# Performance work log

Hardware: AMD Instinct MI355X
Metric: run time of the kernel (lower is better)

The kernel has to match this reference:

```python
import jax, jax.numpy as jnp
import numpy as np

N_NODES = 100000
N_EDGES = 1600000
IN_DIM = 128
OUT_DIM = 64
SLOPE = 0.2


def setup_inputs() -> dict:
    key = jax.random.key(0)
    k1, k2, k3, k4 = jax.random.split(key, 4)
    h = jax.random.normal(k1, (N_NODES, IN_DIM), dtype=jnp.float32)
    W = jax.random.normal(k2, (OUT_DIM, IN_DIM), dtype=jnp.float32) * (1.0 / np.sqrt(IN_DIM))
    src = jax.random.randint(k3, (N_EDGES,), 0, N_NODES, dtype=jnp.int64)
    dst = jax.random.randint(k4, (N_EDGES,), 0, N_NODES, dtype=jnp.int64)
    return {"h": h, "W": W, "src": src, "dst": dst}


def reference(h, W, src, dst):
    n = h.shape[0]
    z = h @ W.T                                   # [N, out_dim]
    z_src = z[src]                                # [E, out_dim]
    z_dst = z[dst]                                # [E, out_dim]
    e = jax.nn.leaky_relu(jnp.sum(z_src * z_dst, axis=1), negative_slope=SLOPE)  # [E]
    # segment softmax over incoming edges of each destination node
    m = jax.ops.segment_max(e, dst, num_segments=n)        # [N], -inf for isolated nodes
    ex = jnp.exp(e - m[dst])                                # [E]
    denom = jax.ops.segment_sum(ex, dst, num_segments=n)    # [N]
    alpha = ex / denom[dst]                                 # [E]
    agg = jax.ops.segment_sum(alpha[:, None] * z_src, dst, num_segments=n)  # [N, out_dim]
    return jax.nn.elu(agg)
```

## Files before the change

### kernel.cpp

```cpp
#include <hip/hip_runtime.h>
#include <math.h>

#define SLOPE 0.2f
#define LOG2E 1.4426950408889634f

__global__ __launch_bounds__(256, 8) void gemm_hist_kernel(const float* __restrict__ h,
                                                           const float* __restrict__ W,
                                                           float* __restrict__ z,
                                                           const int* __restrict__ dst,
                                                           int* __restrict__ cnt8,
                                                           unsigned short* __restrict__ rank,
                                                           int n, int ne) {
    int g = blockIdx.x / 3;
    int r = blockIdx.x % 3;
    if (r == 2) {
        int* __restrict__ cnt = cnt8 + (size_t)(g & 7) * n;
        int i = g * 256 + threadIdx.x;
        int base = i * 4;
        if (base + 3 < ne) {
            int4 d = *(const int4*)(dst + base);
            unsigned int r0 = atomicAdd(&cnt[d.x], 1);
            unsigned int r1 = atomicAdd(&cnt[d.y], 1);
            unsigned int r2 = atomicAdd(&cnt[d.z], 1);
            unsigned int r3 = atomicAdd(&cnt[d.w], 1);
            uint2 packed;
            packed.x = (r1 << 16) | (r0 & 0xFFFF);
            packed.y = (r3 << 16) | (r2 & 0xFFFF);
            *(uint2*)(rank + base) = packed;
        } else if (base < ne) {
            for (int rr = base; rr < ne; rr++)
                rank[rr] = (unsigned short)atomicAdd(&cnt[dst[rr]], 1);
        }
        return;
    }

    __shared__ float ws[128][36];
    int t = threadIdx.x;
    int gemmIdx = 2 * g + r;
    int nblk = gemmIdx >> 1;
    int ch0  = (gemmIdx & 1) << 5;
    const float4* __restrict__ W4 = reinterpret_cast<const float4*>(W);
#pragma unroll
    for (int j = 0; j < 4; j++) {
        int idx = t + j * 256;
        int o  = idx >> 5;
        int kq = idx & 31;
        float4 w = W4[(size_t)(ch0 + o) * 32 + kq];
        int k = kq << 2;
        int col = o ^ ((kq & 7) << 2);
        ws[k + 0][col] = w.x; ws[k + 1][col] = w.y;
        ws[k + 2][col] = w.z; ws[k + 3][col] = w.w;
    }
    __syncthreads();

    int ng = t >> 3, og = t & 7;
    int n0 = nblk * 64 + ng * 2;
    if (n0 >= n) return;
    const float* __restrict__ hp = h + (size_t)n0 * 128;

    float acc[2][4] = {};
#pragma unroll 4
    for (int k = 0; k < 128; k += 4) {
        int m = (k >> 2) & 7;
        int colb = (og ^ m) << 2;
        float4 hv[2], wv[4];
#pragma unroll
        for (int i = 0; i < 2; i++) hv[i] = *(const float4*)(hp + i * 128 + k);
#pragma unroll
        for (int kk = 0; kk < 4; kk++) wv[kk] = *(const float4*)&ws[k + kk][colb];
#pragma unroll
        for (int i = 0; i < 2; i++) {
            acc[i][0] += hv[i].x * wv[0].x + hv[i].y * wv[1].x + hv[i].z * wv[2].x + hv[i].w * wv[3].x;
            acc[i][1] += hv[i].x * wv[0].y + hv[i].y * wv[1].y + hv[i].z * wv[2].y + hv[i].w * wv[3].y;
            acc[i][2] += hv[i].x * wv[0].z + hv[i].y * wv[1].z + hv[i].z * wv[2].z + hv[i].w * wv[3].z;
            acc[i][3] += hv[i].x * wv[0].w + hv[i].y * wv[1].w + hv[i].z * wv[2].w + hv[i].w * wv[3].w;
        }
    }
#pragma unroll
    for (int i = 0; i < 2; i++) {
        *(float4*)&z[(size_t)(n0 + i) * 64 + ch0 + og * 4] =
            make_float4(acc[i][0], acc[i][1], acc[i][2], acc[i][3]);
    }
}

__global__ __launch_bounds__(256) void scan1(const int* __restrict__ cnt8,
                                             int* __restrict__ starts,
                                             int* __restrict__ bsums, int n) {
    __shared__ int ls[256];
    int tbase = blockIdx.x * 4096 + threadIdx.x * 16;
    int tot[16];
#pragma unroll
    for (int k = 0; k < 16; k++) tot[k] = 0;
    if (tbase + 15 < n) {
#pragma unroll
        for (int c = 0; c < 8; c++) {
            const int* cp = cnt8 + (size_t)c * n + tbase;
#pragma unroll
            for (int q = 0; q < 4; q++) {
                int4 v = *(const int4*)(cp + q * 4);
                tot[q * 4 + 0] += v.x; tot[q * 4 + 1] += v.y;
                tot[q * 4 + 2] += v.z; tot[q * 4 + 3] += v.w;
            }
        }
    } else {
        for (int k = 0; k < 16; k++) {
            int idx = tbase + k;
            if (idx < n)
                for (int c = 0; c < 8; c++) tot[k] += cnt8[(size_t)c * n + idx];
        }
    }
    int s = 0;
#pragma unroll
    for (int k = 0; k < 16; k++) s += tot[k];
    ls[threadIdx.x] = s;
    __syncthreads();
    for (int off = 1; off < 256; off <<= 1) {
        int t = threadIdx.x >= off ? ls[threadIdx.x - off] : 0;
        __syncthreads();
        ls[threadIdx.x] += t;
        __syncthreads();
    }
    int run = ls[threadIdx.x] - s;
    if (threadIdx.x == 255) bsums[blockIdx.x] = ls[255];
#pragma unroll
    for (int k = 0; k < 16; k++) {
        int idx = tbase + k;
        if (idx < n) starts[idx] = run;
        run += tot[k];
    }
}

__global__ __launch_bounds__(256) void scan3(int* __restrict__ starts,
                                             const int* __restrict__ bsums,
                                             int* __restrict__ cnt8,
                                             int n, int ne) {
    __shared__ int base_s;
    int i = blockIdx.x * 256 + threadIdx.x;
    if (threadIdx.x == 0) {
        int reg = (int)(blockIdx.x >> 4);
        int s = 0;
        for (int b = 0; b < reg; b++) s += bsums[b];
        base_s = s;
        if (blockIdx.x == 0) starts[n] = ne;
    }
    __syncthreads();
    if (i >= n) return;
    int b = starts[i] + base_s;
    starts[i] = b;
#pragma unroll
    for (int c = 0; c < 8; c++) {
        size_t off = (size_t)c * n + i;
        int t = cnt8[off];
        cnt8[off] = b;
        b += t;
    }
}

__global__ __launch_bounds__(256) void scatter8_kernel(const int* __restrict__ src,
                                                       const int* __restrict__ dst,
                                                       const int* __restrict__ cnt8,
                                                       const unsigned short* __restrict__ rank,
                                                       int* __restrict__ csr_src,
                                                       int n, int ne) {
    int i = blockIdx.x * 256 + threadIdx.x;
    int base = i * 8;
    if (base + 7 < ne) {
        const int* __restrict__ cb = cnt8 + (size_t)((base >> 10) & 7) * n;
        int4 s0 = *(const int4*)(src + base),  s1 = *(const int4*)(src + base + 4);
        int4 d0 = *(const int4*)(dst + base),  d1 = *(const int4*)(dst + base + 4);
        uint4 rp = *(const uint4*)(rank + base);
        csr_src[cb[d0.x] + (rp.x & 0xFFFF)] = s0.x;
        csr_src[cb[d0.y] + (rp.x >> 16)]    = s0.y;
        csr_src[cb[d0.z] + (rp.y & 0xFFFF)] = s0.z;
        csr_src[cb[d0.w] + (rp.y >> 16)]    = s0.w;
        csr_src[cb[d1.x] + (rp.z & 0xFFFF)] = s1.x;
        csr_src[cb[d1.y] + (rp.z >> 16)]    = s1.y;
        csr_src[cb[d1.z] + (rp.w & 0xFFFF)] = s1.z;
        csr_src[cb[d1.w] + (rp.w >> 16)]    = s1.w;
    } else {
        for (int e = base; e < ne; e++) {
            const int* cb = cnt8 + (size_t)((e >> 10) & 7) * n;
            csr_src[cb[dst[e]] + rank[e]] = src[e];
        }
    }
}

__global__ __launch_bounds__(256) void fused_node(const float4* __restrict__ z4,
                                                  const int* __restrict__ starts,
                                                  const int* __restrict__ csr_src,
                                                  float4* __restrict__ out4, int n) {
    int node = blockIdx.x * 4 + (threadIdx.x >> 6);
    if (node >= n) return;
    int lane = threadIdx.x & 63;
    int g = lane >> 4;
    int q = lane & 15;
    int rs = starts[node], re = starts[node + 1];
    float4 zd = z4[(size_t)node * 16 + q];

    float m2 = -1e30f, denom = 0.f;
    float4 acc = make_float4(0.f, 0.f, 0.f, 0.f);

    for (int c = rs; c < re; c += 64) {
        int j = c + lane;
        int sv = j < re ? csr_src[j] : 0;
        int cn = min(64, re - c);
        bool val0 = g < cn;
        int  s0 = __shfl(sv, val0 ? g : 0);
        float4 v0 = z4[(size_t)s0 * 16 + q];
        bool val1 = 4 + g < cn;
        int  s1 = __shfl(sv, val1 ? 4 + g : 0);
        float4 v1 = z4[(size_t)s1 * 16 + q];
        for (int k = 0; k < cn; k += 4) {
            int idx2 = k + 8 + g;
            bool val2 = idx2 < cn;
            int  s2 = __shfl(sv, val2 ? idx2 : 0);
            float4 v2 = z4[(size_t)s2 * 16 + q];
            float p = v0.x * zd.x + v0.y * zd.y + v0.z * zd.z + v0.w * zd.w;
#pragma unroll
            for (int msk = 1; msk < 16; msk <<= 1) p += __shfl_xor(p, msk);
            float e = p > 0.f ? p : SLOPE * p;
            float e2 = e * LOG2E;
            e2 = val0 ? e2 : -2e30f;
            if (__any(e2 > m2)) {
                float mnew = fmaxf(m2, e2);
                float sc = exp2f(m2 - mnew);
                float ex = exp2f(e2 - mnew);
                denom = fmaf(denom, sc, ex);
                acc.x = fmaf(acc.x, sc, ex * v0.x);
                acc.y = fmaf(acc.y, sc, ex * v0.y);
                acc.z = fmaf(acc.z, sc, ex * v0.z);
                acc.w = fmaf(acc.w, sc, ex * v0.w);
                m2 = mnew;
            } else {
                float ex = exp2f(e2 - m2);
                denom += ex;
                acc.x = fmaf(ex, v0.x, acc.x);
                acc.y = fmaf(ex, v0.y, acc.y);
                acc.z = fmaf(ex, v0.z, acc.z);
                acc.w = fmaf(ex, v0.w, acc.w);
            }
            v0 = v1; val0 = val1;
            v1 = v2; val1 = val2;
        }
    }
#pragma unroll
    for (int msk = 16; msk < 64; msk <<= 1) {
        float mo  = __shfl_xor(m2, msk);
        float dno = __shfl_xor(denom, msk);
        float ax = __shfl_xor(acc.x, msk);
        float ay = __shfl_xor(acc.y, msk);
        float az = __shfl_xor(acc.z, msk);
        float aw = __shfl_xor(acc.w, msk);
        float mnew = fmaxf(m2, mo);
        float ss = exp2f(m2 - mnew), so = exp2f(mo - mnew);
        denom = fmaf(denom, ss, dno * so);
        acc.x = fmaf(acc.x, ss, ax * so);
        acc.y = fmaf(acc.y, ss, ay * so);
        acc.z = fmaf(acc.z, ss, az * so);
        acc.w = fmaf(acc.w, ss, aw * so);
        m2 = mnew;
    }
    if (lane < 16) {
        float inv = denom > 0.f ? 1.f / denom : 0.f;
        float4 r; float x;
        x = acc.x * inv; r.x = x > 0.f ? x : __expf(x) - 1.f;
        x = acc.y * inv; r.y = x > 0.f ? x : __expf(x) - 1.f;
        x = acc.z * inv; r.z = x > 0.f ? x : __expf(x) - 1.f;
        x = acc.w * inv; r.w = x > 0.f ? x : __expf(x) - 1.f;
        out4[(size_t)node * 16 + q] = r;
    }
}

extern "C" void kernel_launch(void* const* d_in, const int* in_sizes, int n_in,
                              void* d_out, int out_size, void* d_ws, size_t ws_size,
                              hipStream_t stream) {
    const float* h   = (const float*)d_in[0];
    const float* W   = (const float*)d_in[1];
    const int*   src = (const int*)d_in[2];
    const int*   dst = (const int*)d_in[3];
    int n  = in_sizes[0] / 128;
    int ne = in_sizes[2];

    float*          z       = (float*)d_ws;
    unsigned short* rank    = (unsigned short*)(z + (size_t)n * 64);
    int*            cnt8    = (int*)(rank + ne);
    int*            csr_src = cnt8 + (size_t)8 * n;
    int*            starts  = csr_src + ne;
    int*            bsums   = starts + ((n + 5) & ~3);

    int nbHist = (ne / 4 + 255) / 256;
    int nbTotal = nbHist * 3;
    int nb_scan = (n + 4095) / 4096;

    hipMemsetAsync(cnt8, 0, (size_t)8 * n * sizeof(int), stream);
    gemm_hist_kernel<<<nbTotal, 256, 0, stream>>>(h, W, z, dst, cnt8, rank, n, ne);
    scan1<<<nb_scan, 256, 0, stream>>>(cnt8, starts, bsums, n);
    scan3<<<(n + 255) / 256, 256, 0, stream>>>(starts, bsums, cnt8, n, ne);
    scatter8_kernel<<<(ne / 8 + 255) / 256, 256, 0, stream>>>(src, dst, cnt8,
                                                              rank, csr_src, n, ne);
    fused_node<<<(n + 3) / 4, 256, 0, stream>>>((const float4*)z, starts, csr_src,
                                                (float4*)d_out, n);
}
```

Measured before the change: 196.8 us.

## Store projected features as fp16 and gather eight edges per wavefront step

The GEMM now writes z in half precision, halving the bytes of the intermediate feature table. The node kernel gathers 16-byte fp16 rows with 8 lanes per edge, so each wavefront processes 8 edges per iteration instead of 4 and needs fewer shuffle reductions. This targets the gather bandwidth and instruction count of the random edge reads. In exchange it adds conversion work and rounds z to fp16, which may affect accuracy.

```diff
diff --git a/kernel.cpp b/kernel.cpp
--- a/kernel.cpp
+++ b/kernel.cpp
@@ -1,12 +1,21 @@
 #include <hip/hip_runtime.h>
+#include <hip/hip_fp16.h>
 #include <math.h>
 
 #define SLOPE 0.2f
 #define LOG2E 1.4426950408889634f
 
+__device__ __forceinline__ unsigned short pk_f16(float x) {
+    __half h = __float2half(x);
+    return __half_as_ushort(h);
+}
+__device__ __forceinline__ float f16f(unsigned int bits_lo16) {
+    return __half2float(__ushort_as_half((unsigned short)(bits_lo16 & 0xFFFFu)));
+}
+
 __global__ __launch_bounds__(256, 8) void gemm_hist_kernel(const float* __restrict__ h,
                                                            const float* __restrict__ W,
-                                                           float* __restrict__ z,
+                                                           unsigned short* __restrict__ zh,
                                                            const int* __restrict__ dst,
                                                            int* __restrict__ cnt8,
                                                            unsigned short* __restrict__ rank,
@@ -78,8 +87,12 @@
     }
 #pragma unroll
     for (int i = 0; i < 2; i++) {
-        *(float4*)&z[(size_t)(n0 + i) * 64 + ch0 + og * 4] =
-            make_float4(acc[i][0], acc[i][1], acc[i][2], acc[i][3]);
+        ushort4 o4;
+        o4.x = pk_f16(acc[i][0]);
+        o4.y = pk_f16(acc[i][1]);
+        o4.z = pk_f16(acc[i][2]);
+        o4.w = pk_f16(acc[i][3]);
+        *(ushort4*)&zh[(size_t)(n0 + i) * 64 + ch0 + og * 4] = o4;
     }
 }
 
@@ -185,20 +198,26 @@
     }
 }
 
-__global__ __launch_bounds__(256) void fused_node(const float4* __restrict__ z4,
+__global__ __launch_bounds__(256) void fused_node(const uint4* __restrict__ zh4,
                                                   const int* __restrict__ starts,
                                                   const int* __restrict__ csr_src,
                                                   float4* __restrict__ out4, int n) {
     int node = blockIdx.x * 4 + (threadIdx.x >> 6);
     if (node >= n) return;
     int lane = threadIdx.x & 63;
-    int g = lane >> 4;
-    int q = lane & 15;
+    int g = lane >> 3;
+    int q = lane & 7;
     int rs = starts[node], re = starts[node + 1];
-    float4 zd = z4[(size_t)node * 16 + q];
+
+    uint4 zw = zh4[(size_t)node * 8 + q];
+    float zdf[8];
+    zdf[0] = f16f(zw.x); zdf[1] = f16f(zw.x >> 16);
+    zdf[2] = f16f(zw.y); zdf[3] = f16f(zw.y >> 16);
+    zdf[4] = f16f(zw.z); zdf[5] = f16f(zw.z >> 16);
+    zdf[6] = f16f(zw.w); zdf[7] = f16f(zw.w >> 16);
 
     float m2 = -1e30f, denom = 0.f;
-    float4 acc = make_float4(0.f, 0.f, 0.f, 0.f);
+    float acc[8] = {};
 
     for (int c = rs; c < re; c += 64) {
         int j = c + lane;
@@ -206,18 +225,28 @@
         int cn = min(64, re - c);
         bool val0 = g < cn;
         int  s0 = __shfl(sv, val0 ? g : 0);
-        float4 v0 = z4[(size_t)s0 * 16 + q];
-        bool val1 = 4 + g < cn;
-        int  s1 = __shfl(sv, val1 ? 4 + g : 0);
-        float4 v1 = z4[(size_t)s1 * 16 + q];
-        for (int k = 0; k < cn; k += 4) {
-            int idx2 = k + 8 + g;
+        uint4 w0 = zh4[(size_t)s0 * 8 + q];
+        bool val1 = 8 + g < cn;
+        int  s1 = __shfl(sv, val1 ? 8 + g : 0);
+        uint4 w1 = zh4[(size_t)s1 * 8 + q];
+        for (int k = 0; k < cn; k += 8) {
+            int idx2 = k + 16 + g;
             bool val2 = idx2 < cn;
             int  s2 = __shfl(sv, val2 ? idx2 : 0);
-            float4 v2 = z4[(size_t)s2 * 16 + q];
-            float p = v0.x * zd.x + v0.y * zd.y + v0.z * zd.z + v0.w * zd.w;
-#pragma unroll
-            for (int msk = 1; msk < 16; msk <<= 1) p += __shfl_xor(p, msk);
+            uint4 w2 = zh4[(size_t)s2 * 8 + q];
+
+            float vf[8];
+            vf[0] = f16f(w0.x); vf[1] = f16f(w0.x >> 16);
+            vf[2] = f16f(w0.y); vf[3] = f16f(w0.y >> 16);
+            vf[4] = f16f(w0.z); vf[5] = f16f(w0.z >> 16);
+            vf[6] = f16f(w0.w); vf[7] = f16f(w0.w >> 16);
+
+            float p = vf[0] * zdf[0];
+#pragma unroll
+            for (int jj = 1; jj < 8; jj++) p = fmaf(vf[jj], zdf[jj], p);
+#pragma unroll
+            for (int msk = 1; msk < 8; msk <<= 1) p += __shfl_xor(p, msk);
+
             float e = p > 0.f ? p : SLOPE * p;
             float e2 = e * LOG2E;
             e2 = val0 ? e2 : -2e30f;
@@ -226,48 +255,46 @@
                 float sc = exp2f(m2 - mnew);
                 float ex = exp2f(e2 - mnew);
                 denom = fmaf(denom, sc, ex);
-                acc.x = fmaf(acc.x, sc, ex * v0.x);
-                acc.y = fmaf(acc.y, sc, ex * v0.y);
-                acc.z = fmaf(acc.z, sc, ex * v0.z);
-                acc.w = fmaf(acc.w, sc, ex * v0.w);
+#pragma unroll
+                for (int jj = 0; jj < 8; jj++)
+                    acc[jj] = fmaf(acc[jj], sc, ex * vf[jj]);
                 m2 = mnew;
             } else {
                 float ex = exp2f(e2 - m2);
                 denom += ex;
-                acc.x = fmaf(ex, v0.x, acc.x);
-                acc.y = fmaf(ex, v0.y, acc.y);
-                acc.z = fmaf(ex, v0.z, acc.z);
-                acc.w = fmaf(ex, v0.w, acc.w);
+#pragma unroll
+                for (int jj = 0; jj < 8; jj++)
+                    acc[jj] = fmaf(ex, vf[jj], acc[jj]);
             }
-            v0 = v1; val0 = val1;
-            v1 = v2; val1 = val2;
-        }
-    }
-#pragma unroll
-    for (int msk = 16; msk < 64; msk <<= 1) {
+            w0 = w1; val0 = val1;
+            w1 = w2; val1 = val2;
+        }
+    }
+#pragma unroll
+    for (int msk = 8; msk < 64; msk <<= 1) {
         float mo  = __shfl_xor(m2, msk);
         float dno = __shfl_xor(denom, msk);
-        float ax = __shfl_xor(acc.x, msk);
-        float ay = __shfl_xor(acc.y, msk);
-        float az = __shfl_xor(acc.z, msk);
-        float aw = __shfl_xor(acc.w, msk);
+        float ao[8];
+#pragma unroll
+        for (int jj = 0; jj < 8; jj++) ao[jj] = __shfl_xor(acc[jj], msk);
         float mnew = fmaxf(m2, mo);
         float ss = exp2f(m2 - mnew), so = exp2f(mo - mnew);
         denom = fmaf(denom, ss, dno * so);
-        acc.x = fmaf(acc.x, ss, ax * so);
-        acc.y = fmaf(acc.y, ss, ay * so);
-        acc.z = fmaf(acc.z, ss, az * so);
-        acc.w = fmaf(acc.w, ss, aw * so);
+#pragma unroll
+        for (int jj = 0; jj < 8; jj++)
+            acc[jj] = fmaf(acc[jj], ss, ao[jj] * so);
         m2 = mnew;
     }
-    if (lane < 16) {
+    if (g == 0) {
         float inv = denom > 0.f ? 1.f / denom : 0.f;
-        float4 r; float x;
-        x = acc.x * inv; r.x = x > 0.f ? x : __expf(x) - 1.f;
-        x = acc.y * inv; r.y = x > 0.f ? x : __expf(x) - 1.f;
-        x = acc.z * inv; r.z = x > 0.f ? x : __expf(x) - 1.f;
-        x = acc.w * inv; r.w = x > 0.f ? x : __expf(x) - 1.f;
-        out4[(size_t)node * 16 + q] = r;
+        float r[8];
+#pragma unroll
+        for (int jj = 0; jj < 8; jj++) {
+            float x = acc[jj] * inv;
+            r[jj] = x > 0.f ? x : __expf(x) - 1.f;
+        }
+        out4[(size_t)node * 16 + q * 2 + 0] = make_float4(r[0], r[1], r[2], r[3]);
+        out4[(size_t)node * 16 + q * 2 + 1] = make_float4(r[4], r[5], r[6], r[7]);
     }
 }
 
@@ -281,8 +308,8 @@
     int n  = in_sizes[0] / 128;
     int ne = in_sizes[2];
 
-    float*          z       = (float*)d_ws;
-    unsigned short* rank    = (unsigned short*)(z + (size_t)n * 64);
+    unsigned short* zh      = (unsigned short*)d_ws;
+    unsigned short* rank    = zh + (size_t)n * 64;
     int*            cnt8    = (int*)(rank + ne);
     int*            csr_src = cnt8 + (size_t)8 * n;
     int*            starts  = csr_src + ne;
@@ -293,11 +320,11 @@
     int nb_scan = (n + 4095) / 4096;
 
     hipMemsetAsync(cnt8, 0, (size_t)8 * n * sizeof(int), stream);
-    gemm_hist_kernel<<<nbTotal, 256, 0, stream>>>(h, W, z, dst, cnt8, rank, n, ne);
+    gemm_hist_kernel<<<nbTotal, 256, 0, stream>>>(h, W, zh, dst, cnt8, rank, n, ne);
     scan1<<<nb_scan, 256, 0, stream>>>(cnt8, starts, bsums, n);
     scan3<<<(n + 255) / 256, 256, 0, stream>>>(starts, bsums, cnt8, n, ne);
     scatter8_kernel<<<(ne / 8 + 255) / 256, 256, 0, stream>>>(src, dst, cnt8,
                                                               rank, csr_src, n, ne);
-    fused_node<<<(n + 3) / 4, 256, 0, stream>>>((const float4*)z, starts, csr_src,
+    fused_node<<<(n + 3) / 4, 256, 0, stream>>>((const uint4*)zh, starts, csr_src,
                                                 (float4*)d_out, n);
 }
```

New measurement: 192.0 us. 2.4% less time.
